# Performance work log

Hardware: AMD Instinct MI355X
Metric: run time of the kernel (lower is better)

## Reference

```python
import jax, jax.numpy as jnp
import numpy as np

HEADS = 16
DIM_HEAD = 72
RETAIN_RATE = 0.4


def setup_inputs() -> dict:
    key = jax.random.key(0)
    ks = jax.random.split(key, 6)
    B, N, D = 1, 4096, 1152
    s = D ** -0.5  # keep pre-softmax logits in a sane range
    x = jax.random.normal(ks[0], (B, N, D), dtype=jnp.float32)
    Wq = jax.random.normal(ks[1], (D, D), dtype=jnp.float32) * s
    Wk = jax.random.normal(ks[2], (D, D), dtype=jnp.float32) * s
    Wv = jax.random.normal(ks[3], (D, D), dtype=jnp.float32) * s
    Wo = jax.random.normal(ks[4], (D, D), dtype=jnp.float32) * s
    bo = jnp.zeros((D,), dtype=jnp.float32)
    return {"x": x, "Wq": Wq, "Wk": Wk, "Wv": Wv, "Wo": Wo, "bo": bo}


def reference(x, Wq, Wk, Wv, Wo, bo):
    B, N, D = x.shape
    h, dh = HEADS, DIM_HEAD
    scale = dh ** -0.5

    def split_heads(t):  # [B,N,h*dh] -> [B,h,N,dh]
        return t.reshape(B, N, h, dh).transpose(0, 2, 1, 3)

    q = split_heads(x @ Wq)
    k = split_heads(x @ Wk)
    v = split_heads(x @ Wv)

    sim = jnp.einsum("bhid,bhjd->bhij", q, k) * scale  # [B,h,N,N]
    sim = jax.nn.softmax(sim, axis=-1)

    # ---- PageRank-style power-iteration token importance (apply_wpr path) ----
    attn = sim.mean(axis=1)  # [B,N,N], mean over heads
    dist = jnp.full((B, 1, N), 1.0 / N, dtype=attn.dtype)
    for _ in range(5):  # dist @ attn^5
        dist = dist @ attn
    importance = dist.reshape(B, N)

    k_retain = int(N * RETAIN_RATE)
    _, imp_inds = jax.lax.top_k(importance, k_retain)
    _, prune_inds = jax.lax.top_k(-importance, N - k_retain)
    # torch masked-select gathers rows in ascending index order
    imp_sorted = jnp.sort(imp_inds, axis=1)        # [B, k_retain]
    prune_sorted = jnp.sort(prune_inds, axis=1)    # [B, N-k_retain]
    selected_rows = jnp.take_along_axis(attn, imp_sorted[:, :, None], axis=1)  # [B,k_retain,N]
    max_inds = jnp.argmax(selected_rows, axis=1)   # [B,N] retained-row index with max attention per column
    sim_inds = jnp.take_along_axis(max_inds, prune_sorted, axis=1)  # [B, N-k_retain]

    # ---- standard attention output ----
    out = jnp.einsum("bhij,bhjd->bhid", sim, v)    # [B,h,N,dh]
    out = out.transpose(0, 2, 1, 3).reshape(B, N, h * dh)
    out = out @ Wo + bo
    return out, importance, imp_sorted, prune_sorted, sim_inds
```

## Files before the change

### kernel.cpp

```cpp
#include <hip/hip_runtime.h>
#include <math.h>

#define NT 4096
#define DM 1152
#define NH 16
#define DH 72
#define KRET 1638
#define NPR (NT - KRET)
#define CSB 8
#define ACSB 16
#define CHUNK 205
#define SCALE 0.11785113019775793f
#define RSPLIT 2048.0f
#define INV_RSPLIT 4.8828125e-4f

typedef __attribute__((ext_vector_type(8))) short bf16x8;
typedef _Float16 f16;
typedef __attribute__((ext_vector_type(8))) _Float16 f16x8;
typedef __attribute__((ext_vector_type(4))) float f32x4;
typedef unsigned short ushort_t;

#define MFMA16(a, b, c) __builtin_amdgcn_mfma_f32_16x16x32_f16(a, b, c, 0, 0, 0)
#define MFMABF(a, b, c) __builtin_amdgcn_mfma_f32_16x16x32_bf16(a, b, c, 0, 0, 0)

__device__ inline ushort_t f2b(float f) {
    union { float f; unsigned int u; } v; v.f = f;
    unsigned int u = v.u;
    return (ushort_t)((u + 0x7FFFu + ((u >> 16) & 1u)) >> 16);
}

__device__ inline size_t qkAddr(int h, int row, int ks, int ki) {
    return ((((size_t)h * 256 + (row >> 4)) * 3 + ks) * 16 + (row & 15)) * 32 + ki;
}

__global__ __launch_bounds__(256) void split_x(
    const float* __restrict__ in, f16* __restrict__ x0, f16* __restrict__ x1,
    ushort_t* __restrict__ xb, int nElem)
{
    int i = blockIdx.x * 256 + threadIdx.x;
    int stride = gridDim.x * 256;
    for (; i < nElem; i += stride) {
        float v = in[i];
        f16 h0 = (f16)v;
        float res = (v - (float)h0) * RSPLIT;
        x0[i] = h0;
        x1[i] = (f16)res;
        xb[i] = f2b(v);
    }
}

__global__ __launch_bounds__(256) void transposeW_split(
    const float* __restrict__ W, f16* __restrict__ T0, f16* __restrict__ T1, int n)
{
    __shared__ float t[32][33];
    int bx = blockIdx.x * 32, by = blockIdx.y * 32;
    int tx = threadIdx.x & 31, ty = threadIdx.x >> 5;
    for (int i = ty; i < 32; i += 8)
        t[i][tx] = W[(size_t)(by + i) * n + bx + tx];
    __syncthreads();
    for (int i = ty; i < 32; i += 8) {
        float v = t[tx][i];
        f16 h0 = (f16)v;
        float res = (v - (float)h0) * RSPLIT;
        T0[(size_t)(bx + i) * n + by + tx] = h0;
        T1[(size_t)(bx + i) * n + by + tx] = (f16)res;
    }
}

__global__ __launch_bounds__(256) void transposeW_bf16(
    const float* __restrict__ W, ushort_t* __restrict__ WT, int n)
{
    __shared__ ushort_t t[32][33];
    int bx = blockIdx.x * 32, by = blockIdx.y * 32;
    int tx = threadIdx.x & 31, ty = threadIdx.x >> 5;
    for (int i = ty; i < 32; i += 8)
        t[i][tx] = f2b(W[(size_t)(by + i) * n + bx + tx]);
    __syncthreads();
    for (int i = ty; i < 32; i += 8)
        WT[(size_t)(bx + i) * n + by + tx] = t[tx][i];
}

__global__ __launch_bounds__(256) void proj_split3(
    const f16* __restrict__ A0, const f16* __restrict__ A1,
    const f16* __restrict__ B0, const f16* __restrict__ B1,
    f16* __restrict__ Qt0, f16* __restrict__ Qt1, float scl)
{
    __shared__ __align__(16) f16 As0[128][40];
    __shared__ __align__(16) f16 As1[128][40];
    __shared__ __align__(16) f16 Bs0[64][40];
    __shared__ __align__(16) f16 Bs1[64][40];
    const int tid = threadIdx.x;
    const int wave = tid >> 6, lane = tid & 63;
    const int r = lane & 15, g = lane >> 4;
    const int row0 = blockIdx.y * 128;
    const int col0 = blockIdx.x * 64;
    f32x4 accM[2][4] = {}, accC[2][4] = {};
    for (int k0 = 0; k0 < DM; k0 += 32) {
        for (int idx = tid; idx < 128 * 4; idx += 256) {
            int row = idx >> 2, c = idx & 3;
            size_t src = (size_t)(row0 + row) * DM + k0 + c * 8;
            *(f16x8*)&As0[row][c * 8] = *(const f16x8*)(A0 + src);
            *(f16x8*)&As1[row][c * 8] = *(const f16x8*)(A1 + src);
        }
        for (int idx = tid; idx < 64 * 4; idx += 256) {
            int row = idx >> 2, c = idx & 3;
            size_t src = (size_t)(col0 + row) * DM + k0 + c * 8;
            *(f16x8*)&Bs0[row][c * 8] = *(const f16x8*)(B0 + src);
            *(f16x8*)&Bs1[row][c * 8] = *(const f16x8*)(B1 + src);
        }
        __syncthreads();
        f16x8 a0[2], a1[2], b0[4], b1[4];
#pragma unroll
        for (int rf = 0; rf < 2; ++rf) {
            a0[rf] = *(const f16x8*)&As0[wave * 32 + rf * 16 + r][g * 8];
            a1[rf] = *(const f16x8*)&As1[wave * 32 + rf * 16 + r][g * 8];
        }
#pragma unroll
        for (int cf = 0; cf < 4; ++cf) {
            b0[cf] = *(const f16x8*)&Bs0[cf * 16 + r][g * 8];
            b1[cf] = *(const f16x8*)&Bs1[cf * 16 + r][g * 8];
        }
#pragma unroll
        for (int rf = 0; rf < 2; ++rf)
#pragma unroll
            for (int cf = 0; cf < 4; ++cf) {
                accM[rf][cf] = MFMA16(a0[rf], b0[cf], accM[rf][cf]);
                accC[rf][cf] = MFMA16(a0[rf], b1[cf], accC[rf][cf]);
                accC[rf][cf] = MFMA16(a1[rf], b0[cf], accC[rf][cf]);
            }
        __syncthreads();
    }
#pragma unroll
    for (int rf = 0; rf < 2; ++rf)
#pragma unroll
        for (int cf = 0; cf < 4; ++cf) {
            int col = col0 + cf * 16 + r;
            int head = col / DH;
            int c = col - head * DH;
            int ks = c >> 5, ki = c & 31;
#pragma unroll
            for (int j = 0; j < 4; ++j) {
                int row = row0 + wave * 32 + rf * 16 + g * 4 + j;
                float v = (accM[rf][cf][j] + accC[rf][cf][j] * INV_RSPLIT) * scl;
                f16 h0 = (f16)v;
                float res = (v - (float)h0) * RSPLIT;
                size_t addr = qkAddr(head, row, ks, ki);
                Qt0[addr] = h0;
                Qt1[addr] = (f16)res;
            }
        }
}

__global__ __launch_bounds__(256) void gemm_bf16_lds(
    const ushort_t* __restrict__ A, const ushort_t* __restrict__ BT,
    const float* __restrict__ bias, void* __restrict__ C, int mode,
    int Nn, int K)
{
    __shared__ __align__(16) ushort_t As[128][40];
    __shared__ __align__(16) ushort_t Bs[64][40];
    const int tid = threadIdx.x;
    const int wave = tid >> 6, lane = tid & 63;
    const int r = lane & 15, g = lane >> 4;
    const int row0 = blockIdx.y * 128;
    const int col0 = blockIdx.x * 64;
    f32x4 acc[2][4] = {};
    for (int k0 = 0; k0 < K; k0 += 32) {
        for (int idx = tid; idx < 128 * 4; idx += 256) {
            int row = idx >> 2, c = idx & 3;
            *(bf16x8*)&As[row][c * 8] = *(const bf16x8*)(A + (size_t)(row0 + row) * K + k0 + c * 8);
        }
        for (int idx = tid; idx < 64 * 4; idx += 256) {
            int row = idx >> 2, c = idx & 3;
            *(bf16x8*)&Bs[row][c * 8] = *(const bf16x8*)(BT + (size_t)(col0 + row) * K + k0 + c * 8);
        }
        __syncthreads();
        bf16x8 a[2], b[4];
#pragma unroll
        for (int rf = 0; rf < 2; ++rf)
            a[rf] = *(const bf16x8*)&As[wave * 32 + rf * 16 + r][g * 8];
#pragma unroll
        for (int cf = 0; cf < 4; ++cf)
            b[cf] = *(const bf16x8*)&Bs[cf * 16 + r][g * 8];
#pragma unroll
        for (int rf = 0; rf < 2; ++rf)
#pragma unroll
            for (int cf = 0; cf < 4; ++cf)
                acc[rf][cf] = MFMABF(a[rf], b[cf], acc[rf][cf]);
        __syncthreads();
    }
#pragma unroll
    for (int rf = 0; rf < 2; ++rf)
#pragma unroll
        for (int cf = 0; cf < 4; ++cf) {
            int col = col0 + cf * 16 + r;
            float bv = bias ? bias[col] : 0.f;
#pragma unroll
            for (int j = 0; j < 4; ++j) {
                int row = row0 + wave * 32 + rf * 16 + g * 4 + j;
                float vv = acc[rf][cf][j] + bv;
                if (mode == 2) {
                    int head = col / DH;
                    int d = col - head * DH;
                    size_t addr = (((size_t)head * 128 + (row >> 5)) * 80 + d) * 32 + (row & 31);
                    ((ushort_t*)C)[addr] = f2b(vv);
                } else {
                    ((float*)C)[(size_t)row * Nn + col] = vv;
                }
            }
        }
}

__global__ __launch_bounds__(256) void rowsum_pv(
    const f16* __restrict__ Qt0, const f16* __restrict__ Qt1,
    const f16* __restrict__ Kt0, const f16* __restrict__ Kt1,
    const ushort_t* __restrict__ Vp,
    float* __restrict__ invs, ushort_t* __restrict__ otmpb)
{
    __shared__ __align__(16) f16 KL[2][6144];
    const int tid = threadIdx.x;
    const int wv = tid >> 6, lane = tid & 63;
    const int r = lane & 15, g = lane >> 4;
    const int h = blockIdx.y;
    const int rowblk = blockIdx.x * 4 + wv;
    f16x8 a0[3], a1[3];
#pragma unroll
    for (int ks = 0; ks < 3; ++ks) {
        size_t o = ((((size_t)h * 256 + rowblk) * 3 + ks) * 16) * 32 + r * 32 + g * 8;
        a0[ks] = *(const f16x8*)(Qt0 + o);
        a1[ks] = *(const f16x8*)(Qt1 + o);
    }
    const int c32p0 = ((r >> 2) << 3) + (r & 3);
    float rs = 0.f;
    f32x4 oacc[5] = {};
    for (int ct = 0; ct < 64; ++ct) {
        __syncthreads();
        const size_t ctBase = ((size_t)h * 256 + ct * 4) * 1536;
#pragma unroll
        for (int s = 0; s < 6; ++s) {
            int wc = s * 4 + wv;
            int plane = wc >= 12;
            int cip = wc - plane * 12;
            const f16* src = (plane ? Kt1 : Kt0) + ctBase + cip * 512 + lane * 8;
            *(f16x8*)&KL[plane][cip * 512 + lane * 8] = *(const f16x8*)src;
        }
        __syncthreads();
        f32x4 accM[4] = {}, accC[4] = {};
#pragma unroll
        for (int ks = 0; ks < 3; ++ks) {
#pragma unroll
            for (int group = 0; group < 2; ++group) {
#pragma unroll
                for (int cfp = 0; cfp < 2; ++cfp) {
                    const int c32 = c32p0 + cfp * 4;
                    const int off = (((group * 2 + (c32 >> 4)) * 3 + ks) << 9)
                                  + ((c32 & 15) << 5) + (g << 3);
                    f16x8 b0 = *(const f16x8*)&KL[0][off];
                    f16x8 b1 = *(const f16x8*)&KL[1][off];
                    const int cf = group * 2 + cfp;
                    accM[cf] = MFMA16(b0, a0[ks], accM[cf]);
                    accC[cf] = MFMA16(b1, a0[ks], accC[cf]);
                    accC[cf] = MFMA16(b0, a1[ks], accC[cf]);
                }
            }
        }
        const int kt0 = ct * 2;
#pragma unroll
        for (int group = 0; group < 2; ++group) {
            bf16x8 pa;
#pragma unroll
            for (int cfp = 0; cfp < 2; ++cfp) {
                const int cf = group * 2 + cfp;
#pragma unroll
                for (int j = 0; j < 4; ++j) {
                    float ev = __expf(accM[cf][j] + accC[cf][j] * INV_RSPLIT);
                    rs += ev;
                    pa[cfp * 4 + j] = (short)f2b(ev);
                }
            }
#pragma unroll
            for (int t = 0; t < 5; ++t) {
                int col = t * 16 + r;
                size_t vo = (((size_t)h * 128 + kt0 + group) * 80 + col) * 32 + g * 8;
                bf16x8 b = *(const bf16x8*)(Vp + vo);
                oacc[t] = MFMABF(pa, b, oacc[t]);
            }
        }
    }
    rs += __shfl_xor(rs, 16);
    rs += __shfl_xor(rs, 32);
    const float inv = 1.0f / rs;
    if (g == 0)
        invs[(size_t)h * NT + rowblk * 16 + r] = inv;
    float invq[4];
#pragma unroll
    for (int j = 0; j < 4; ++j) invq[j] = __shfl(inv, g * 4 + j);
#pragma unroll
    for (int t = 0; t < 5; ++t) {
        int col = t * 16 + r;
        if (col < DH) {
#pragma unroll
            for (int j = 0; j < 4; ++j) {
                int row = rowblk * 16 + g * 4 + j;
                otmpb[(size_t)row * DM + h * DH + col] = f2b(oacc[t][j] * invq[j]);
            }
        }
    }
}

__global__ __launch_bounds__(256) void attn_sum(
    const f16* __restrict__ Qt0, const f16* __restrict__ Qt1,
    const f16* __restrict__ Kt0, const f16* __restrict__ Kt1,
    const float* __restrict__ invs, float* __restrict__ attn)
{
    __shared__ __align__(16) f16 KL[2][6144];
    const int tid = threadIdx.x;
    const int wr = tid >> 6, lane = tid & 63;
    const int r = lane & 15, g = lane >> 4;
    const int cs = blockIdx.x;
    const int rowblk = blockIdx.y * 4 + wr;
    const int row0 = rowblk * 16;
    const int cb0 = cs * 16;
    float aacc[4][4][4] = {};
    for (int h = 0; h < NH; ++h) {
        f16x8 a0[3], a1[3];
#pragma unroll
        for (int ks = 0; ks < 3; ++ks) {
            size_t o = ((((size_t)h * 256 + rowblk) * 3 + ks) * 16) * 32 + r * 32 + g * 8;
            a0[ks] = *(const f16x8*)(Qt0 + o);
            a1[ks] = *(const f16x8*)(Qt1 + o);
        }
        float vinv[4];
#pragma unroll
        for (int j = 0; j < 4; ++j)
            vinv[j] = invs[(size_t)h * NT + row0 + g * 4 + j];
#pragma unroll
        for (int ct = 0; ct < 4; ++ct) {
            __syncthreads();
            const size_t ctBase = ((size_t)h * 256 + cb0 + ct * 4) * 1536;
#pragma unroll
            for (int s = 0; s < 6; ++s) {
                int wc = s * 4 + wr;
                int plane = wc >= 12;
                int cip = wc - plane * 12;
                const f16* src = (plane ? Kt1 : Kt0) + ctBase + cip * 512 + lane * 8;
                *(f16x8*)&KL[plane][cip * 512 + lane * 8] = *(const f16x8*)src;
            }
            __syncthreads();
            f32x4 accM[4] = {}, accC[4] = {};
#pragma unroll
            for (int ks = 0; ks < 3; ++ks) {
#pragma unroll
                for (int cf = 0; cf < 4; ++cf) {
                    f16x8 b0 = *(const f16x8*)&KL[0][(cf * 3 + ks) * 512 + r * 32 + g * 8];
                    f16x8 b1 = *(const f16x8*)&KL[1][(cf * 3 + ks) * 512 + r * 32 + g * 8];
                    accM[cf] = MFMA16(a0[ks], b0, accM[cf]);
                    accC[cf] = MFMA16(a0[ks], b1, accC[cf]);
                    accC[cf] = MFMA16(a1[ks], b0, accC[cf]);
                }
            }
#pragma unroll
            for (int cf = 0; cf < 4; ++cf) {
#pragma unroll
                for (int j = 0; j < 4; ++j) {
                    float p = __expf(accM[cf][j] + accC[cf][j] * INV_RSPLIT) * vinv[j];
                    aacc[ct][cf][j] += p;
                }
            }
        }
    }
#pragma unroll
    for (int ct = 0; ct < 4; ++ct) {
        const int colbase = cs * 256 + ct * 64;
#pragma unroll
        for (int cf = 0; cf < 4; ++cf) {
#pragma unroll
            for (int j = 0; j < 4; ++j) {
                int row = row0 + g * 4 + j;
                attn[(size_t)row * NT + colbase + cf * 16 + r] = aacc[ct][cf][j] * 0.0625f;
            }
        }
    }
}

__global__ __launch_bounds__(256) void init_dist(float* __restrict__ d)
{
    int t = blockIdx.x * 256 + threadIdx.x;
    if (t < NT) d[t] = 1.0f / NT;
}

__global__ __launch_bounds__(256) void power_a(
    const float* __restrict__ attn, const float* __restrict__ din,
    float* __restrict__ part)
{
    int j = blockIdx.x * 256 + threadIdx.x;
    int i0 = blockIdx.y * 128;
    float acc = 0.f;
    for (int i = i0; i < i0 + 128; ++i)
        acc += din[i] * attn[(size_t)i * NT + j];
    part[(size_t)blockIdx.y * NT + j] = acc;
}

__global__ __launch_bounds__(256) void power_b(
    const float* __restrict__ part, float* __restrict__ dout)
{
    int j = blockIdx.x * 256 + threadIdx.x;
    float acc = 0.f;
    for (int ib = 0; ib < 32; ++ib) acc += part[(size_t)ib * NT + j];
    dout[j] = acc;
}

__global__ __launch_bounds__(256) void rank_count(
    const float* __restrict__ imp, int* __restrict__ rank, int* __restrict__ prank)
{
    __shared__ float sj[256];
    const int tid = threadIdx.x;
    const int jb = blockIdx.y * 256;
    sj[tid] = imp[jb + tid];
    __syncthreads();
    const int i = blockIdx.x * 256 + tid;
    const float mv = imp[i];
    int r = 0, rp = 0;
    for (int jj = 0; jj < 256; ++jj) {
        float vj = sj[jj];
        int j = jb + jj;
        int tie_low = (vj == mv) && (j < i);
        r  += (vj > mv) || tie_low;
        rp += (vj < mv) || tie_low;
    }
    atomicAdd(&rank[i], r);
    atomicAdd(&prank[i], rp);
}

__global__ __launch_bounds__(256) void scatter_topk2(
    const int* __restrict__ rank, const int* __restrict__ prank,
    float* __restrict__ out_imps, float* __restrict__ out_prune,
    int* __restrict__ imp_rows, int* __restrict__ prune_cols)
{
    __shared__ unsigned char fr[NT];
    __shared__ unsigned char fp[NT];
    __shared__ int sr[256], sp[256];
    const int tid = threadIdx.x;
    for (int t = tid; t < NT; t += 256) {
        fr[t] = rank[t] < KRET;
        fp[t] = prank[t] < NPR;
    }
    __syncthreads();
    const int base = tid * 16;
    int cr = 0, cp = 0;
#pragma unroll
    for (int e = 0; e < 16; ++e) { cr += fr[base + e]; cp += fp[base + e]; }
    sr[tid] = cr; sp[tid] = cp;
    __syncthreads();
    int pr = 0, pp = 0;
    for (int j = 0; j < tid; ++j) { pr += sr[j]; pp += sp[j]; }
#pragma unroll
    for (int e = 0; e < 16; ++e) {
        int i = base + e;
        if (fr[i]) { out_imps[pr] = (float)i; imp_rows[pr] = i; ++pr; }
        if (fp[i]) { out_prune[pp] = (float)i; prune_cols[pp] = i; ++pp; }
    }
}

__global__ __launch_bounds__(256) void argmax_part(
    const float* __restrict__ attn, const int* __restrict__ imp_rows,
    float* __restrict__ pbest, int* __restrict__ pbi)
{
    __shared__ int rows[CHUNK];
    const int tid = threadIdx.x;
    const int rc = blockIdx.y;
    const int r0 = rc * CHUNK;
    const int nr = min(KRET - r0, CHUNK);
    for (int t = tid; t < nr; t += 256) rows[t] = imp_rows[r0 + t];
    __syncthreads();
    const int j = blockIdx.x * 256 + tid;
    float best = -INFINITY;
    int bi = 0;
    for (int rr = 0; rr < nr; ++rr) {
        float val = attn[(size_t)rows[rr] * NT + j];
        if (val > best) { best = val; bi = r0 + rr; }
    }
    pbest[(size_t)rc * NT + j] = best;
    pbi[(size_t)rc * NT + j] = bi;
}

__global__ __launch_bounds__(256) void argmax_red(
    const float* __restrict__ pbest, const int* __restrict__ pbi,
    int* __restrict__ maxind)
{
    const int j = blockIdx.x * 256 + threadIdx.x;
    float best = -INFINITY;
    int bi = 0;
#pragma unroll
    for (int rc = 0; rc < 8; ++rc) {
        float val = pbest[(size_t)rc * NT + j];
        if (val > best) { best = val; bi = pbi[(size_t)rc * NT + j]; }
    }
    maxind[j] = bi;
}

__global__ __launch_bounds__(256) void finalize(
    const float* __restrict__ dist, const int* __restrict__ prune_cols,
    const int* __restrict__ maxind, float* __restrict__ out_imp,
    float* __restrict__ out_simi)
{
    int t = blockIdx.x * 256 + threadIdx.x;
    if (t < NT) out_imp[t] = dist[t];
    if (t < NPR) out_simi[t] = (float)maxind[prune_cols[t]];
}

extern "C" void kernel_launch(void* const* d_in, const int* in_sizes, int n_in,
                              void* d_out, int out_size, void* d_ws, size_t ws_size,
                              hipStream_t stream)
{
    const float* x  = (const float*)d_in[0];
    const float* Wq = (const float*)d_in[1];
    const float* Wk = (const float*)d_in[2];
    const float* Wv = (const float*)d_in[3];
    const float* Wo = (const float*)d_in[4];
    const float* bo = (const float*)d_in[5];
    float* out = (float*)d_out;

    const size_t QKT_EL = (size_t)NH * 256 * 3 * 16 * 32;
    const size_t VP_EL  = (size_t)NH * 128 * 80 * 32;

    float* ws = (float*)d_ws;
    size_t off = 0;
    float* attn = ws + off; off += (size_t)NT * NT;
    f16* Qt0 = (f16*)(ws + off); off += QKT_EL / 2;
    f16* Qt1 = (f16*)(ws + off); off += QKT_EL / 2;
    f16* Kt0 = (f16*)(ws + off); off += QKT_EL / 2;
    f16* Kt1 = (f16*)(ws + off); off += QKT_EL / 2;
    ushort_t* Vp = (ushort_t*)(ws + off); off += VP_EL / 2;
    size_t zero_floats = 4 * (QKT_EL / 2) + VP_EL / 2;
    ushort_t* otmpb = (ushort_t*)(ws + off); off += ((size_t)NT * DM) / 2;
    f16* X0 = (f16*)(ws + off); f16* X1 = X0 + (size_t)NT * DM; off += (size_t)NT * DM;
    f16* T0 = (f16*)(ws + off); f16* T1 = T0 + (size_t)DM * DM; off += (size_t)DM * DM;
    ushort_t* Wslot = (ushort_t*)(ws + off); off += ((size_t)DM * DM) / 2;
    float* invs    = ws + off; off += (size_t)NH * NT;
    float* pbest   = ws + off; off += 8 * NT;
    int*   pbi     = (int*)(ws + off); off += 8 * NT;
    float* dist0 = ws + off; off += NT;
    float* dist1 = ws + off; off += NT;
    float* partial = ws + off; off += 32 * NT;
    int* rank      = (int*)(ws + off); off += NT;
    int* prank     = (int*)(ws + off); off += NT;
    int* imp_rows  = (int*)(ws + off); off += 2048;
    int* prune_cols= (int*)(ws + off); off += 2560;
    int* maxind    = (int*)(ws + off); off += NT;

    ushort_t* xb = (ushort_t*)attn;

    float* out_out   = out;
    float* out_imp   = out + (size_t)NT * DM;
    float* out_imps  = out_imp + NT;
    float* out_prune = out_imps + KRET;
    float* out_simi  = out_prune + NPR;

    hipMemsetAsync(Qt0, 0, zero_floats * sizeof(float), stream);
    split_x<<<2048, 256, 0, stream>>>(x, X0, X1, xb, NT * DM);

    dim3 gT(DM / 32, DM / 32);
    dim3 gP(DM / 64, NT / 128);
    transposeW_split<<<gT, 256, 0, stream>>>(Wq, T0, T1, DM);
    proj_split3<<<gP, 256, 0, stream>>>(X0, X1, T0, T1, Qt0, Qt1, SCALE);
    transposeW_split<<<gT, 256, 0, stream>>>(Wk, T0, T1, DM);
    proj_split3<<<gP, 256, 0, stream>>>(X0, X1, T0, T1, Kt0, Kt1, 1.0f);

    transposeW_bf16<<<gT, 256, 0, stream>>>(Wv, Wslot, DM);
    gemm_bf16_lds<<<gP, 256, 0, stream>>>(xb, Wslot, nullptr, Vp, 2, DM, DM);

    rowsum_pv<<<dim3(NT / 64, NH), 256, 0, stream>>>(Qt0, Qt1, Kt0, Kt1, Vp,
                                                     invs, otmpb);

    attn_sum<<<dim3(ACSB, NT / 64), 256, 0, stream>>>(Qt0, Qt1, Kt0, Kt1, invs, attn);

    transposeW_bf16<<<gT, 256, 0, stream>>>(Wo, Wslot, DM);
    gemm_bf16_lds<<<gP, 256, 0, stream>>>(otmpb, Wslot, bo, out_out, 0, DM, DM);

    init_dist<<<16, 256, 0, stream>>>(dist0);
    float* da = dist0;
    float* db = dist1;
    for (int it = 0; it < 5; ++it) {
        power_a<<<dim3(16, 32), 256, 0, stream>>>(attn, da, partial);
        power_b<<<16, 256, 0, stream>>>(partial, db);
        float* t = da; da = db; db = t;
    }

    hipMemsetAsync(rank, 0, 2 * NT * sizeof(int), stream);
    rank_count<<<dim3(16, 16), 256, 0, stream>>>(da, rank, prank);
    scatter_topk2<<<1, 256, 0, stream>>>(rank, prank, out_imps, out_prune,
                                         imp_rows, prune_cols);
    argmax_part<<<dim3(16, 8), 256, 0, stream>>>(attn, imp_rows, pbest, pbi);
    argmax_red<<<16, 256, 0, stream>>>(pbest, pbi, maxind);
    finalize<<<16, 256, 0, stream>>>(da, prune_cols, maxind, out_imp, out_simi);
}
```

Baseline: 930.1 us.

## Split rowsum_pv across key halves and narrow attn_sum column tiles

The softmax row-sum plus PV kernel is now split over two halves of the key range (grid z=2), writing partial row sums and partial unnormalised PV in bf16. A new pv_norm kernel combines the halves, forms the inverse row sums and writes the normalised output. attn_sum's column-block count is doubled with half the columns per block, cutting per-thread accumulators. This raises occupancy and grid size (the old grid was only 1024 blocks) at the cost of an extra kernel, extra global traffic, and an added bf16 rounding of the partial PV sums.

```diff
diff --git a/kernel.cpp b/kernel.cpp
--- a/kernel.cpp
+++ b/kernel.cpp
@@ -7,8 +7,7 @@
 #define DH 72
 #define KRET 1638
 #define NPR (NT - KRET)
-#define CSB 8
-#define ACSB 16
+#define ACSB 32
 #define CHUNK 205
 #define SCALE 0.11785113019775793f
 #define RSPLIT 2048.0f
@@ -27,6 +26,11 @@
     union { float f; unsigned int u; } v; v.f = f;
     unsigned int u = v.u;
     return (ushort_t)((u + 0x7FFFu + ((u >> 16) & 1u)) >> 16);
+}
+
+__device__ inline float b2f(ushort_t u) {
+    union { unsigned int u; float f; } v; v.u = ((unsigned int)u) << 16;
+    return v.f;
 }
 
 __device__ inline size_t qkAddr(int h, int row, int ks, int ki) {
@@ -214,13 +218,14 @@
     const f16* __restrict__ Qt0, const f16* __restrict__ Qt1,
     const f16* __restrict__ Kt0, const f16* __restrict__ Kt1,
     const ushort_t* __restrict__ Vp,
-    float* __restrict__ invs, ushort_t* __restrict__ otmpb)
+    float* __restrict__ rsPart, ushort_t* __restrict__ part_pv)
 {
     __shared__ __align__(16) f16 KL[2][6144];
     const int tid = threadIdx.x;
     const int wv = tid >> 6, lane = tid & 63;
     const int r = lane & 15, g = lane >> 4;
     const int h = blockIdx.y;
+    const int half = blockIdx.z;
     const int rowblk = blockIdx.x * 4 + wv;
     f16x8 a0[3], a1[3];
 #pragma unroll
@@ -232,7 +237,7 @@
     const int c32p0 = ((r >> 2) << 3) + (r & 3);
     float rs = 0.f;
     f32x4 oacc[5] = {};
-    for (int ct = 0; ct < 64; ++ct) {
+    for (int ct = half * 32; ct < half * 32 + 32; ++ct) {
         __syncthreads();
         const size_t ctBase = ((size_t)h * 256 + ct * 4) * 1536;
 #pragma unroll
@@ -288,12 +293,8 @@
     }
     rs += __shfl_xor(rs, 16);
     rs += __shfl_xor(rs, 32);
-    const float inv = 1.0f / rs;
     if (g == 0)
-        invs[(size_t)h * NT + rowblk * 16 + r] = inv;
-    float invq[4];
-#pragma unroll
-    for (int j = 0; j < 4; ++j) invq[j] = __shfl(inv, g * 4 + j);
+        rsPart[((size_t)half * NH + h) * NT + rowblk * 16 + r] = rs;
 #pragma unroll
     for (int t = 0; t < 5; ++t) {
         int col = t * 16 + r;
@@ -301,9 +302,34 @@
 #pragma unroll
             for (int j = 0; j < 4; ++j) {
                 int row = rowblk * 16 + g * 4 + j;
-                otmpb[(size_t)row * DM + h * DH + col] = f2b(oacc[t][j] * invq[j]);
-            }
-        }
+                part_pv[(((size_t)half * NH + h) * NT + row) * DH + col] = f2b(oacc[t][j]);
+            }
+        }
+    }
+}
+
+__global__ __launch_bounds__(256) void pv_norm(
+    const float* __restrict__ rsPart, const ushort_t* __restrict__ part_pv,
+    float* __restrict__ invs, ushort_t* __restrict__ otmpb)
+{
+    __shared__ float sinv[32];
+    const int h = blockIdx.x;
+    const int row0 = blockIdx.y * 32;
+    const int tid = threadIdx.x;
+    if (tid < 32) {
+        float rsA = rsPart[(size_t)h * NT + row0 + tid];
+        float rsB = rsPart[((size_t)NH + h) * NT + row0 + tid];
+        float inv = 1.0f / (rsA + rsB);
+        sinv[tid] = inv;
+        invs[(size_t)h * NT + row0 + tid] = inv;
+    }
+    __syncthreads();
+    for (int e = tid; e < 32 * DH; e += 256) {
+        int rr = e / DH, col = e - rr * DH;
+        int row = row0 + rr;
+        float a = b2f(part_pv[((size_t)h * NT + row) * DH + col]);
+        float b = b2f(part_pv[(((size_t)NH + h) * NT + row) * DH + col]);
+        otmpb[(size_t)row * DM + h * DH + col] = f2b((a + b) * sinv[rr]);
     }
 }
 
@@ -319,8 +345,8 @@
     const int cs = blockIdx.x;
     const int rowblk = blockIdx.y * 4 + wr;
     const int row0 = rowblk * 16;
-    const int cb0 = cs * 16;
-    float aacc[4][4][4] = {};
+    const int cb0 = cs * 8;
+    float aacc[2][4][4] = {};
     for (int h = 0; h < NH; ++h) {
         f16x8 a0[3], a1[3];
 #pragma unroll
@@ -334,7 +360,7 @@
         for (int j = 0; j < 4; ++j)
             vinv[j] = invs[(size_t)h * NT + row0 + g * 4 + j];
 #pragma unroll
-        for (int ct = 0; ct < 4; ++ct) {
+        for (int ct = 0; ct < 2; ++ct) {
             __syncthreads();
             const size_t ctBase = ((size_t)h * 256 + cb0 + ct * 4) * 1536;
 #pragma unroll
@@ -369,8 +395,8 @@
         }
     }
 #pragma unroll
-    for (int ct = 0; ct < 4; ++ct) {
-        const int colbase = cs * 256 + ct * 64;
+    for (int ct = 0; ct < 2; ++ct) {
+        const int colbase = cs * 128 + ct * 64;
 #pragma unroll
         for (int cf = 0; cf < 4; ++cf) {
 #pragma unroll
@@ -537,6 +563,8 @@
     f16* T0 = (f16*)(ws + off); f16* T1 = T0 + (size_t)DM * DM; off += (size_t)DM * DM;
     ushort_t* Wslot = (ushort_t*)(ws + off); off += ((size_t)DM * DM) / 2;
     float* invs    = ws + off; off += (size_t)NH * NT;
+    float* rsPart  = ws + off; off += (size_t)2 * NH * NT;
+    ushort_t* part_pv = (ushort_t*)(ws + off); off += (size_t)2 * NH * NT * DH / 2;
     float* pbest   = ws + off; off += 8 * NT;
     int*   pbi     = (int*)(ws + off); off += 8 * NT;
     float* dist0 = ws + off; off += NT;
@@ -569,8 +597,9 @@
     transposeW_bf16<<<gT, 256, 0, stream>>>(Wv, Wslot, DM);
     gemm_bf16_lds<<<gP, 256, 0, stream>>>(xb, Wslot, nullptr, Vp, 2, DM, DM);
 
-    rowsum_pv<<<dim3(NT / 64, NH), 256, 0, stream>>>(Qt0, Qt1, Kt0, Kt1, Vp,
-                                                     invs, otmpb);
+    rowsum_pv<<<dim3(NT / 64, NH, 2), 256, 0, stream>>>(Qt0, Qt1, Kt0, Kt1, Vp,
+                                                        rsPart, part_pv);
+    pv_norm<<<dim3(NH, NT / 32), 256, 0, stream>>>(rsPart, part_pv, invs, otmpb);
 
     attn_sum<<<dim3(ACSB, NT / 64), 256, 0, stream>>>(Qt0, Qt1, Kt0, Kt1, invs, attn);
 
```

Result: faster. 843.3 us (-9.3%).
